# Optimization experiments

Measured on AMD Instinct MI355X. Metric: run time of the kernel, lower is better.

The kernel has to match this reference:

```python
import jax, jax.numpy as jnp
import numpy as np

SIGMA = 5.67e-8  # Stefan-Boltzmann constant
NX = 13
N = NX * NX  # 169 nodes
B = 131072


def _build_matrices(L=0.1, thickness=0.001, board_k=15.0, emis=0.8):
    dx = L / (NX - 1)
    dy = L / (NX - 1)
    GLx = thickness * board_k * dy / dx
    GLy = thickness * board_k * dx / dy
    GR = 2.0 * dx * dy * emis
    iface = {0, NX - 1, NX * NX - 1, NX * NX - NX}
    K = np.zeros((N, N), dtype=np.float32)
    for j in range(NX):
        for i in range(NX):
            idn = i + NX * j
            if idn in iface:
                K[idn, idn] = 1.0
            else:
                gii = 0.0
                if i + 1 < NX:
                    K[idn, idn + 1] = -GLx  # east
                    gii += GLx
                if i - 1 >= 0:
                    K[idn, idn - 1] = -GLx  # west
                    gii += GLx
                if j + 1 < NX:
                    K[idn, idn + NX] = -GLx  # north (original code uses -GLx here too)
                    gii += GLy
                if j - 1 >= 0:
                    K[idn, idn - NX] = -GLx  # south (original code uses -GLx here too)
                    gii += GLy
                K[idn, idn] = gii
    e = np.full(N, GR, dtype=np.float32)
    for t in iface:
        e[t] = 0.0
    return jnp.asarray(K), jnp.asarray(e)


def setup_inputs() -> dict:
    key = jax.random.key(0)
    k1, k2, k3, k4 = jax.random.split(key, 4)
    # realistic temperatures (K) and heat loads (W)
    outputs = 270.0 + 60.0 * jax.random.uniform(k1, (B, NX, NX), dtype=jnp.float32)
    heaters = 0.5 * jax.random.uniform(k2, (B, NX, NX), dtype=jnp.float32)
    interfaces = 0.5 * jax.random.uniform(k3, (B, NX, NX), dtype=jnp.float32)
    Tenv = 270.0 + 30.0 * jax.random.uniform(k4, (B, 1), dtype=jnp.float32)
    K, e_diag = _build_matrices()
    return {"outputs": outputs, "heaters": heaters, "interfaces": interfaces,
            "Tenv": Tenv, "K": K, "e_diag": e_diag}


def reference(outputs, heaters, interfaces, Tenv, K, e_diag):
    b = outputs.shape[0]
    T = outputs.reshape(b, -1)                    # [B, 169]
    Q = heaters.reshape(b, -1) + interfaces.reshape(b, -1)  # [B, 169]
    # original computes K @ T_nodes_x_batch; batch-major equivalent is T @ K^T
    conduction = jnp.einsum('bn,mn->bm', T, K)    # [B, 169]
    radiation = SIGMA * e_diag[None, :] * (T ** 4 - Tenv ** 4)  # Tenv [B,1] broadcasts
    excess = conduction + radiation - Q
    return jnp.mean(jnp.abs(excess))
```

## Files before the change

### kernel.cpp

```cpp
#include <hip/hip_runtime.h>
#include <math.h>


#define SIGMA_F 5.67e-8f

constexpr int BLOCK = 256;

typedef float f4a __attribute__((ext_vector_type(4), aligned(4)));

__global__ __launch_bounds__(256) void fused_residual_v5(
    const float* __restrict__ T,
    const float* __restrict__ H,
    const float* __restrict__ F,
    const float* __restrict__ Tenv,
    const float* __restrict__ K,
    const float* __restrict__ Ediag,
    float* __restrict__ partials,
    int rows)
{
    __shared__ float sred[BLOCK / 64];

    const float GLx = -K[1 * 169 + 2];
    const float GRs = SIGMA_F * Ediag[1];

    float acc = 0.0f;

    const int gstride = gridDim.x * BLOCK;
    for (int r = blockIdx.x * BLOCK + (int)threadIdx.x; r < rows; r += gstride) {
        const unsigned ur = (unsigned)r;
        const unsigned b  = ur / 13u;
        const int j = (int)(ur - b * 13u);
        const bool cS = (j > 0), cN = (j < 12);
        const float fS = cS ? 1.0f : 0.0f;
        const float fN = cN ? 1.0f : 0.0f;

        const int e0 = r * 13;
        const float* Tp = T + e0;
        const float* Sp = T + (cS ? e0 - 13 : e0);
        const float* Np = T + (cN ? e0 + 13 : e0);

        f4a tA = *(const f4a*)(Tp);
        f4a tB = *(const f4a*)(Tp + 4);
        f4a tC = *(const f4a*)(Tp + 8);
        float t12 = Tp[12];
        f4a sA = *(const f4a*)(Sp);
        f4a sB = *(const f4a*)(Sp + 4);
        f4a sC = *(const f4a*)(Sp + 8);
        float s12 = Sp[12];
        f4a nA = *(const f4a*)(Np);
        f4a nB = *(const f4a*)(Np + 4);
        f4a nC = *(const f4a*)(Np + 8);
        float n12 = Np[12];
        f4a hA = __builtin_nontemporal_load((const f4a*)(H + e0));
        f4a hB = __builtin_nontemporal_load((const f4a*)(H + e0 + 4));
        f4a hC = __builtin_nontemporal_load((const f4a*)(H + e0 + 8));
        float h12 = __builtin_nontemporal_load(H + e0 + 12);
        f4a fA = __builtin_nontemporal_load((const f4a*)(F + e0));
        f4a fB = __builtin_nontemporal_load((const f4a*)(F + e0 + 4));
        f4a fC = __builtin_nontemporal_load((const f4a*)(F + e0 + 8));
        float f12 = __builtin_nontemporal_load(F + e0 + 12);

        const float tv  = Tenv[b];
        const float tv2 = tv * tv;
        const float nGtv4 = -(GRs * (tv2 * tv2));

        const float tR[13] = {tA.x, tA.y, tA.z, tA.w, tB.x, tB.y, tB.z, tB.w,
                              tC.x, tC.y, tC.z, tC.w, t12};
        const float sR[13] = {sA.x, sA.y, sA.z, sA.w, sB.x, sB.y, sB.z, sB.w,
                              sC.x, sC.y, sC.z, sC.w, s12};
        const float nR[13] = {nA.x, nA.y, nA.z, nA.w, nB.x, nB.y, nB.z, nB.w,
                              nC.x, nC.y, nC.z, nC.w, n12};
        const float qR[13] = {hA.x + fA.x, hA.y + fA.y, hA.z + fA.z, hA.w + fA.w,
                              hB.x + fB.x, hB.y + fB.y, hB.z + fB.z, hB.w + fB.w,
                              hC.x + fC.x, hC.y + fC.y, hC.z + fC.z, hC.w + fC.w,
                              h12 + f12};

        const float nnI = 2.0f + fN + fS;
        const float nnE = 1.0f + fN + fS;
        const bool ifc = (j == 0) | (j == 12);

        {
            float t = tR[0];
            float s = tR[1];
            s = fmaf(fN, nR[0], s);
            s = fmaf(fS, sR[0], s);
            float t2 = t * t;
            float ex = fmaf(GLx, fmaf(nnE, t, -s), fmaf(GRs, t2 * t2, nGtv4)) - qR[0];
            float exI = t - qR[0];
            acc += fabsf(ifc ? exI : ex);
        }
        #pragma unroll
        for (int i = 1; i < 12; ++i) {
            float t = tR[i];
            float s = tR[i - 1] + tR[i + 1];
            s = fmaf(fN, nR[i], s);
            s = fmaf(fS, sR[i], s);
            float t2 = t * t;
            float ex = fmaf(GLx, fmaf(nnI, t, -s), fmaf(GRs, t2 * t2, nGtv4)) - qR[i];
            acc += fabsf(ex);
        }
        {
            float t = tR[12];
            float s = tR[11];
            s = fmaf(fN, nR[12], s);
            s = fmaf(fS, sR[12], s);
            float t2 = t * t;
            float ex = fmaf(GLx, fmaf(nnE, t, -s), fmaf(GRs, t2 * t2, nGtv4)) - qR[12];
            float exI = t - qR[12];
            acc += fabsf(ifc ? exI : ex);
        }
    }

    #pragma unroll
    for (int off = 32; off > 0; off >>= 1)
        acc += __shfl_down(acc, off, 64);
    const int lane = threadIdx.x & 63;
    const int wid  = threadIdx.x >> 6;
    if (lane == 0) sred[wid] = acc;
    __syncthreads();
    if (threadIdx.x == 0) {
        float s = 0.0f;
        #pragma unroll
        for (int w = 0; w < BLOCK / 64; ++w) s += sred[w];
        partials[blockIdx.x] = s;
    }
}

__global__ __launch_bounds__(256) void finalize_kernel(
    const float* __restrict__ partials, int n,
    float* __restrict__ out, float inv_total)
{
    __shared__ float sred[BLOCK / 64];
    float acc = 0.0f;
    for (int i = (int)threadIdx.x; i < n; i += BLOCK) acc += partials[i];
    #pragma unroll
    for (int off = 32; off > 0; off >>= 1)
        acc += __shfl_down(acc, off, 64);
    int lane = threadIdx.x & 63;
    int wid  = threadIdx.x >> 6;
    if (lane == 0) sred[wid] = acc;
    __syncthreads();
    if (threadIdx.x == 0) {
        float s = 0.0f;
        #pragma unroll
        for (int w = 0; w < BLOCK / 64; ++w) s += sred[w];
        out[0] = s * inv_total;
    }
}

extern "C" void kernel_launch(void* const* d_in, const int* in_sizes, int n_in,
                              void* d_out, int out_size, void* d_ws, size_t ws_size,
                              hipStream_t stream) {
    const float* T    = (const float*)d_in[0];
    const float* H    = (const float*)d_in[1];
    const float* F    = (const float*)d_in[2];
    const float* Tenv = (const float*)d_in[3];
    const float* K    = (const float*)d_in[4];
    const float* E    = (const float*)d_in[5];
    float* out      = (float*)d_out;
    float* partials = (float*)d_ws;

    const int total = in_sizes[0];
    const int rows  = total / 13;

    int grid = (rows + BLOCK - 1) / BLOCK;
    if ((size_t)grid * sizeof(float) > ws_size) grid = (int)(ws_size / sizeof(float));
    if (grid < 1) grid = 1;

    fused_residual_v5<<<grid, BLOCK, 0, stream>>>(T, H, F, Tenv, K, E, partials, rows);

    const float inv_total = 1.0f / (float)total;
    finalize_kernel<<<1, BLOCK, 0, stream>>>(partials, grid, out, inv_total);
}
```

Measured before the change: 275.0 us.

## Stage T and Q tiles in shared memory with coalesced vector loads

Each block now copies a contiguous window of T (with a 16-float halo on each side) and the pre-summed H+F into LDS using aligned 16-byte coalesced loads, then each thread reads its row and its north/south neighbours from LDS. This replaces per-thread strided unaligned 13-float global loads, which read each T row three times. The cost is about 27 KB of LDS per block, which may limit occupancy, plus extra barriers and LDS reads with a 13-float stride that can cause bank conflicts.

```diff
diff --git a/kernel.cpp b/kernel.cpp
--- a/kernel.cpp
+++ b/kernel.cpp
@@ -5,10 +5,12 @@
 #define SIGMA_F 5.67e-8f
 
 constexpr int BLOCK = 256;
+constexpr int TWIN  = 3360;
+constexpr int QWIN  = 3328;
 
-typedef float f4a __attribute__((ext_vector_type(4), aligned(4)));
+typedef float f4 __attribute__((ext_vector_type(4), aligned(16)));
 
-__global__ __launch_bounds__(256) void fused_residual_v5(
+__global__ __launch_bounds__(256) void fused_residual_v6(
     const float* __restrict__ T,
     const float* __restrict__ H,
     const float* __restrict__ F,
@@ -16,109 +18,119 @@
     const float* __restrict__ K,
     const float* __restrict__ Ediag,
     float* __restrict__ partials,
-    int rows)
+    int rows,
+    int total)
 {
+    __shared__ float sT[TWIN];
+    __shared__ float sQ[QWIN];
     __shared__ float sred[BLOCK / 64];
 
     const float GLx = -K[1 * 169 + 2];
     const float GRs = SIGMA_F * Ediag[1];
+    const int tid = (int)threadIdx.x;
 
     float acc = 0.0f;
 
-    const int gstride = gridDim.x * BLOCK;
-    for (int r = blockIdx.x * BLOCK + (int)threadIdx.x; r < rows; r += gstride) {
-        const unsigned ur = (unsigned)r;
-        const unsigned b  = ur / 13u;
-        const int j = (int)(ur - b * 13u);
-        const bool cS = (j > 0), cN = (j < 12);
-        const float fS = cS ? 1.0f : 0.0f;
-        const float fN = cN ? 1.0f : 0.0f;
+    for (int blk = (int)blockIdx.x; blk * BLOCK < rows; blk += (int)gridDim.x) {
+        const int r0 = blk * BLOCK;
+        const int e0 = r0 * 13;
+        const int ws = e0 - 16;
 
-        const int e0 = r * 13;
-        const float* Tp = T + e0;
-        const float* Sp = T + (cS ? e0 - 13 : e0);
-        const float* Np = T + (cN ? e0 + 13 : e0);
+        if (blk != (int)blockIdx.x) __syncthreads();
 
-        f4a tA = *(const f4a*)(Tp);
-        f4a tB = *(const f4a*)(Tp + 4);
-        f4a tC = *(const f4a*)(Tp + 8);
-        float t12 = Tp[12];
-        f4a sA = *(const f4a*)(Sp);
-        f4a sB = *(const f4a*)(Sp + 4);
-        f4a sC = *(const f4a*)(Sp + 8);
-        float s12 = Sp[12];
-        f4a nA = *(const f4a*)(Np);
-        f4a nB = *(const f4a*)(Np + 4);
-        f4a nC = *(const f4a*)(Np + 8);
-        float n12 = Np[12];
-        f4a hA = __builtin_nontemporal_load((const f4a*)(H + e0));
-        f4a hB = __builtin_nontemporal_load((const f4a*)(H + e0 + 4));
-        f4a hC = __builtin_nontemporal_load((const f4a*)(H + e0 + 8));
-        float h12 = __builtin_nontemporal_load(H + e0 + 12);
-        f4a fA = __builtin_nontemporal_load((const f4a*)(F + e0));
-        f4a fB = __builtin_nontemporal_load((const f4a*)(F + e0 + 4));
-        f4a fC = __builtin_nontemporal_load((const f4a*)(F + e0 + 8));
-        float f12 = __builtin_nontemporal_load(F + e0 + 12);
+        const bool fast = (ws >= 0) && (ws + TWIN <= total);
+        if (fast) {
+            #pragma unroll
+            for (int it = 0; it < 4; ++it) {
+                const int idx = tid + it * BLOCK;
+                if (idx < TWIN / 4) {
+                    f4 v = *(const f4*)(T + ws + idx * 4);
+                    *(f4*)(sT + idx * 4) = v;
+                }
+                if (idx < QWIN / 4) {
+                    f4 h = __builtin_nontemporal_load((const f4*)(H + e0 + idx * 4));
+                    f4 f = __builtin_nontemporal_load((const f4*)(F + e0 + idx * 4));
+                    *(f4*)(sQ + idx * 4) = h + f;
+                }
+            }
+        } else {
+            for (int k = tid; k < TWIN; k += BLOCK) {
+                int g = ws + k;
+                g = g < 0 ? 0 : (g >= total ? total - 1 : g);
+                sT[k] = T[g];
+            }
+            for (int k = tid; k < QWIN; k += BLOCK) {
+                int g = e0 + k;
+                sQ[k] = (g < total) ? (H[g] + F[g]) : 0.0f;
+            }
+        }
+        __syncthreads();
 
-        const float tv  = Tenv[b];
-        const float tv2 = tv * tv;
-        const float nGtv4 = -(GRs * (tv2 * tv2));
+        const int r = r0 + tid;
+        if (r < rows) {
+            const unsigned b = (unsigned)r / 13u;
+            const int j = r - (int)(b * 13u);
+            const float fS = (j > 0)  ? 1.0f : 0.0f;
+            const float fN = (j < 12) ? 1.0f : 0.0f;
+            const bool ifc = (j == 0) | (j == 12);
 
-        const float tR[13] = {tA.x, tA.y, tA.z, tA.w, tB.x, tB.y, tB.z, tB.w,
-                              tC.x, tC.y, tC.z, tC.w, t12};
-        const float sR[13] = {sA.x, sA.y, sA.z, sA.w, sB.x, sB.y, sB.z, sB.w,
-                              sC.x, sC.y, sC.z, sC.w, s12};
-        const float nR[13] = {nA.x, nA.y, nA.z, nA.w, nB.x, nB.y, nB.z, nB.w,
-                              nC.x, nC.y, nC.z, nC.w, n12};
-        const float qR[13] = {hA.x + fA.x, hA.y + fA.y, hA.z + fA.z, hA.w + fA.w,
-                              hB.x + fB.x, hB.y + fB.y, hB.z + fB.z, hB.w + fB.w,
-                              hC.x + fC.x, hC.y + fC.y, hC.z + fC.z, hC.w + fC.w,
-                              h12 + f12};
+            const float tv  = Tenv[b];
+            const float tv2 = tv * tv;
+            const float nGtv4 = -(GRs * (tv2 * tv2));
 
-        const float nnI = 2.0f + fN + fS;
-        const float nnE = 1.0f + fN + fS;
-        const bool ifc = (j == 0) | (j == 12);
+            const int lb = 16 + tid * 13;
 
-        {
-            float t = tR[0];
-            float s = tR[1];
-            s = fmaf(fN, nR[0], s);
-            s = fmaf(fS, sR[0], s);
-            float t2 = t * t;
-            float ex = fmaf(GLx, fmaf(nnE, t, -s), fmaf(GRs, t2 * t2, nGtv4)) - qR[0];
-            float exI = t - qR[0];
-            acc += fabsf(ifc ? exI : ex);
-        }
-        #pragma unroll
-        for (int i = 1; i < 12; ++i) {
-            float t = tR[i];
-            float s = tR[i - 1] + tR[i + 1];
-            s = fmaf(fN, nR[i], s);
-            s = fmaf(fS, sR[i], s);
-            float t2 = t * t;
-            float ex = fmaf(GLx, fmaf(nnI, t, -s), fmaf(GRs, t2 * t2, nGtv4)) - qR[i];
-            acc += fabsf(ex);
-        }
-        {
-            float t = tR[12];
-            float s = tR[11];
-            s = fmaf(fN, nR[12], s);
-            s = fmaf(fS, sR[12], s);
-            float t2 = t * t;
-            float ex = fmaf(GLx, fmaf(nnE, t, -s), fmaf(GRs, t2 * t2, nGtv4)) - qR[12];
-            float exI = t - qR[12];
-            acc += fabsf(ifc ? exI : ex);
+            float tR[13], sv[13], nv[13], qv[13];
+            #pragma unroll
+            for (int i = 0; i < 13; ++i) tR[i] = sT[lb + i];
+            #pragma unroll
+            for (int i = 0; i < 13; ++i) sv[i] = sT[lb - 13 + i];
+            #pragma unroll
+            for (int i = 0; i < 13; ++i) nv[i] = sT[lb + 13 + i];
+            #pragma unroll
+            for (int i = 0; i < 13; ++i) qv[i] = sQ[tid * 13 + i];
+
+            const float nnI = 2.0f + fN + fS;
+            const float nnE = 1.0f + fN + fS;
+
+            {
+                float t = tR[0];
+                float s = tR[1];
+                s = fmaf(fN, nv[0], s);
+                s = fmaf(fS, sv[0], s);
+                float t2 = t * t;
+                float ex = fmaf(GLx, fmaf(nnE, t, -s), fmaf(GRs, t2 * t2, nGtv4)) - qv[0];
+                acc += fabsf(ifc ? (t - qv[0]) : ex);
+            }
+            #pragma unroll
+            for (int i = 1; i < 12; ++i) {
+                float t = tR[i];
+                float s = tR[i - 1] + tR[i + 1];
+                s = fmaf(fN, nv[i], s);
+                s = fmaf(fS, sv[i], s);
+                float t2 = t * t;
+                acc += fabsf(fmaf(GLx, fmaf(nnI, t, -s), fmaf(GRs, t2 * t2, nGtv4)) - qv[i]);
+            }
+            {
+                float t = tR[12];
+                float s = tR[11];
+                s = fmaf(fN, nv[12], s);
+                s = fmaf(fS, sv[12], s);
+                float t2 = t * t;
+                float ex = fmaf(GLx, fmaf(nnE, t, -s), fmaf(GRs, t2 * t2, nGtv4)) - qv[12];
+                acc += fabsf(ifc ? (t - qv[12]) : ex);
+            }
         }
     }
 
     #pragma unroll
     for (int off = 32; off > 0; off >>= 1)
         acc += __shfl_down(acc, off, 64);
-    const int lane = threadIdx.x & 63;
-    const int wid  = threadIdx.x >> 6;
+    const int lane = tid & 63;
+    const int wid  = tid >> 6;
     if (lane == 0) sred[wid] = acc;
     __syncthreads();
-    if (threadIdx.x == 0) {
+    if (tid == 0) {
         float s = 0.0f;
         #pragma unroll
         for (int w = 0; w < BLOCK / 64; ++w) s += sred[w];
@@ -167,7 +179,8 @@
     if ((size_t)grid * sizeof(float) > ws_size) grid = (int)(ws_size / sizeof(float));
     if (grid < 1) grid = 1;
 
-    fused_residual_v5<<<grid, BLOCK, 0, stream>>>(T, H, F, Tenv, K, E, partials, rows);
+    fused_residual_v6<<<grid, BLOCK, 0, stream>>>(T, H, F, Tenv, K, E, partials,
+                                                  rows, total);
 
     const float inv_total = 1.0f / (float)total;
     finalize_kernel<<<1, BLOCK, 0, stream>>>(partials, grid, out, inv_total);
```

New measurement: 258.7 us. 5.9% less time.
